# Performance work log

Hardware: AMD Instinct MI355X
Metric: run time of the kernel (lower is better)

## Reference

```python
import jax, jax.numpy as jnp
import numpy as np

B, N, C, D = 16, 1024, 768, 384

def setup_inputs() -> dict:
    key = jax.random.key(0)
    ks = jax.random.split(key, 12)
    s_in = 1.0 / np.sqrt(C)
    s_d = 1.0 / np.sqrt(D)
    return {
        "x": jax.random.normal(ks[0], (B, N, C), dtype=jnp.float32),
        "adj": jax.random.uniform(ks[1], (B, N, N), dtype=jnp.float32),
        "W_theta": jax.random.uniform(ks[2], (C, D), minval=-s_in, maxval=s_in),
        "b_theta": jax.random.uniform(ks[3], (D,), minval=-s_in, maxval=s_in),
        "W_phi": jax.random.uniform(ks[4], (C, D), minval=-s_in, maxval=s_in),
        "b_phi": jax.random.uniform(ks[5], (D,), minval=-s_in, maxval=s_in),
        "W_g": jax.random.uniform(ks[6], (C, D), minval=-s_in, maxval=s_in),
        "b_g": jax.random.uniform(ks[7], (D,), minval=-s_in, maxval=s_in),
        "W_out": jax.random.uniform(ks[8], (D, C), minval=-s_d, maxval=s_d),
        "b_out": jax.random.uniform(ks[9], (C,), minval=-s_d, maxval=s_d),
    }

def reference(x, adj, W_theta, b_theta, W_phi, b_phi, W_g, b_g, W_out, b_out):
    # projections: [B,N,C] @ [C,D] -> [B,N,D]
    theta = x @ W_theta + b_theta
    phi = x @ W_phi + b_phi
    g = x @ W_g + b_g
    # unscaled attention scores with multiplicative adjacency mask
    attn = jnp.einsum('bnd,bmd->bnm', theta, phi) * adj  # [B,N,N]
    attn = jax.nn.softmax(attn, axis=-1)  # dropout is identity in eval mode
    out = jnp.einsum('bnm,bmd->bnd', attn, g)  # [B,N,D]
    out = out @ W_out + b_out  # [B,N,C]
    return out + x
```

## Files before the change

kernel.cpp:

```cpp
#include <hip/hip_runtime.h>
#include <hip/hip_bf16.h>

typedef __hip_bfloat16 bf16;
typedef short bf16x8 __attribute__((ext_vector_type(8)));
typedef float f32x4 __attribute__((ext_vector_type(4)));

constexpr int Bb = 16, Nn = 1024, Cc = 768, Dd = 384;

static __device__ __forceinline__ f32x4 mfma16(bf16x8 a, bf16x8 b, f32x4 c) {
    return __builtin_amdgcn_mfma_f32_16x16x32_bf16(a, b, c, 0, 0, 0);
}
static __device__ __forceinline__ short f2b(float v) {
    __hip_bfloat16 h = __float2bfloat16(v);
    return *reinterpret_cast<short*>(&h);
}
static __device__ __forceinline__ unsigned pack2(float lo, float hi) {
    return ((unsigned)(unsigned short)f2b(hi) << 16) | (unsigned short)(unsigned)f2b(lo);
}
static __device__ __forceinline__ float b2f(bf16 x) { return __bfloat162float(x); }

__global__ __launch_bounds__(256) void cast_bf16(
    const float* __restrict__ in, uint4* __restrict__ out)
{
    const size_t i = (size_t)blockIdx.x * 256 + threadIdx.x;
    const float4 a = reinterpret_cast<const float4*>(in)[i * 2];
    const float4 b = reinterpret_cast<const float4*>(in)[i * 2 + 1];
    uint4 v;
    v.x = pack2(a.x, a.y);
    v.y = pack2(a.z, a.w);
    v.z = pack2(b.x, b.y);
    v.w = pack2(b.z, b.w);
    out[i] = v;
}

__global__ __launch_bounds__(256) void pack_bias(
    const float* __restrict__ bt, const float* __restrict__ bp,
    const float* __restrict__ bg, float* __restrict__ out)
{
    const int i = blockIdx.x * 256 + threadIdx.x;
    if (i < 384) out[i] = bt[i];
    else if (i < 768) out[i] = bp[i - 384];
    else if (i < 1152) out[i] = bg[i - 768];
}

__global__ __launch_bounds__(256) void transpose_cast(
    const float* __restrict__ in, bf16* __restrict__ out, int K, int N)
{
    __shared__ float t[32][33];
    const int n0 = blockIdx.x * 32, k0 = blockIdx.y * 32;
    const int tx = threadIdx.x & 31, ty = threadIdx.x >> 5;
#pragma unroll
    for (int i = 0; i < 4; i++)
        t[ty + i * 8][tx] = in[(size_t)(k0 + ty + i * 8) * N + n0 + tx];
    __syncthreads();
#pragma unroll
    for (int i = 0; i < 4; i++)
        out[(size_t)(n0 + ty + i * 8) * K + k0 + tx] = __float2bfloat16(t[tx][ty + i * 8]);
}

template <typename TA, int EPI>
__global__ __launch_bounds__(256) void gemm_mfma(
    const TA* __restrict__ A, const bf16* __restrict__ BT,
    const float* __restrict__ bias, const float* __restrict__ resid,
    void* __restrict__ outp, int K, int Nout)
{
    __shared__ short As[128 * 40];
    __shared__ short Bs[128 * 40];
    const int tid = threadIdx.x;
    const int lane = tid & 63, w = tid >> 6;
    const int quad = lane >> 4, c = lane & 15;
    const int row0 = blockIdx.x * 128, col0 = blockIdx.y * 128;
    const int wm = (w & 1) * 64, wn = (w >> 1) * 64;

    const f32x4 fz = {0.f, 0.f, 0.f, 0.f};
    f32x4 acc[4][4];
#pragma unroll
    for (int i = 0; i < 4; i++)
#pragma unroll
        for (int j = 0; j < 4; j++) acc[i][j] = fz;

    for (int k0 = 0; k0 < K; k0 += 32) {
        __syncthreads();
        if (sizeof(TA) == 4) {
            const float* Af = (const float*)A;
#pragma unroll
            for (int u = 0; u < 4; u++) {
                const int id = u * 256 + tid;
                const int r = id >> 3, c4 = (id & 7) * 4;
                const float4 v = *reinterpret_cast<const float4*>(Af + (size_t)(row0 + r) * K + k0 + c4);
                uint2 p;
                p.x = pack2(v.x, v.y);
                p.y = pack2(v.z, v.w);
                *reinterpret_cast<uint2*>(&As[r * 40 + c4]) = p;
            }
        } else {
            const bf16* Ab = (const bf16*)A;
#pragma unroll
            for (int u = 0; u < 2; u++) {
                const int id = u * 256 + tid;
                const int r = id >> 2, c8 = (id & 3) * 8;
                const uint4 v = *reinterpret_cast<const uint4*>(Ab + (size_t)(row0 + r) * K + k0 + c8);
                *reinterpret_cast<uint4*>(&As[r * 40 + c8]) = v;
            }
        }
#pragma unroll
        for (int u = 0; u < 2; u++) {
            const int id = u * 256 + tid;
            const int r = id >> 2, c8 = (id & 3) * 8;
            const uint4 v = *reinterpret_cast<const uint4*>(BT + (size_t)(col0 + r) * K + k0 + c8);
            *reinterpret_cast<uint4*>(&Bs[r * 40 + c8]) = v;
        }
        __syncthreads();

        bf16x8 af[4], bfr[4];
#pragma unroll
        for (int i = 0; i < 4; i++)
            af[i] = *reinterpret_cast<const bf16x8*>(&As[(wm + i * 16 + c) * 40 + quad * 8]);
#pragma unroll
        for (int j = 0; j < 4; j++)
            bfr[j] = *reinterpret_cast<const bf16x8*>(&Bs[(wn + j * 16 + c) * 40 + quad * 8]);
#pragma unroll
        for (int i = 0; i < 4; i++)
#pragma unroll
            for (int j = 0; j < 4; j++)
                acc[i][j] = mfma16(af[i], bfr[j], acc[i][j]);
    }

    const size_t SZc = (size_t)Bb * Nn * Dd;
#pragma unroll
    for (int i = 0; i < 4; i++) {
        const int rowb = row0 + wm + i * 16 + quad * 4;
#pragma unroll
        for (int j = 0; j < 4; j++) {
            const int col = col0 + wn + j * 16 + c;
            const float bcol = bias[col];
#pragma unroll
            for (int r = 0; r < 4; r++) {
                float v = acc[i][j][r] + bcol;
                const int rr = rowb + r;
                if (EPI == 0) {
                    ((bf16*)outp)[(size_t)rr * Nout + col] = __float2bfloat16(v);
                } else if (EPI == 1) {
                    const int bb = rr >> 10, m = rr & 1023;
                    ((bf16*)outp)[((size_t)(bb * Nout + col)) * 1024 + m] = __float2bfloat16(v);
                } else if (EPI == 2) {
                    v += resid[(size_t)rr * Nout + col];
                    ((float*)outp)[(size_t)rr * Nout + col] = v;
                } else {
                    const int seg = col / 384;
                    const int cl = col - seg * 384;
                    bf16* base = (bf16*)outp;
                    if (seg < 2) {
                        base[(size_t)seg * SZc + (size_t)rr * Dd + cl] = __float2bfloat16(v);
                    } else {
                        const int bb = rr >> 10, m = rr & 1023;
                        base[2 * SZc + ((size_t)(bb * Dd + cl)) * 1024 + m] = __float2bfloat16(v);
                    }
                }
            }
        }
    }
}

template <int SPLIT>
__global__ __launch_bounds__(256, 2) void flash_attn(
    const bf16* __restrict__ theta, const bf16* __restrict__ phi,
    const bf16* __restrict__ gT, const float* __restrict__ adj,
    bf16* __restrict__ O, float* __restrict__ Sp, float* __restrict__ ml)
{
    __shared__ short phs[32 * 392];
    __shared__ short gts[384 * 40];
    __shared__ short pls[4][16 * 40];

    const int tid = threadIdx.x;
    const int lane = tid & 63, w = tid >> 6;
    const int quad = lane >> 4, c = lane & 15;
    const int qb = blockIdx.x, b = blockIdx.y;
    const int sp = SPLIT ? blockIdx.z : 0;
    const int n_lo = SPLIT ? sp * (Nn / 2) : 0;
    const int n_hi = SPLIT ? n_lo + Nn / 2 : Nn;

    const size_t thbase = ((size_t)b * Nn + qb * 64 + w * 16 + c) * Dd;
    bf16x8 ath[12];
#pragma unroll
    for (int dq = 0; dq < 12; dq++)
        ath[dq] = *reinterpret_cast<const bf16x8*>(theta + thbase + dq * 32 + quad * 8);

    const f32x4 fz = {0.f, 0.f, 0.f, 0.f};
    f32x4 o[24];
#pragma unroll
    for (int t = 0; t < 24; t++) o[t] = fz;
    float mrow[4], lrow[4];
#pragma unroll
    for (int r = 0; r < 4; r++) { mrow[r] = -INFINITY; lrow[r] = 0.f; }

    for (int n0 = n_lo; n0 < n_hi; n0 += 32) {
        __syncthreads();
        {
            const bf16* src = phi + ((size_t)b * Nn + n0) * Dd;
#pragma unroll
            for (int u = 0; u < 6; u++) {
                const int id = u * 256 + tid;
                const int r = id / 48, cc = (id % 48) * 8;
                const uint4 v = *reinterpret_cast<const uint4*>(src + (size_t)r * Dd + cc);
                *reinterpret_cast<uint4*>(&phs[r * 392 + cc]) = v;
            }
        }
        {
            const bf16* src = gT + ((size_t)b * Dd) * Nn + n0;
#pragma unroll
            for (int u = 0; u < 6; u++) {
                const int id = u * 256 + tid;
                const int r = id >> 2, cc = (id & 3) * 8;
                const uint4 v = *reinterpret_cast<const uint4*>(src + (size_t)r * Nn + cc);
                *reinterpret_cast<uint4*>(&gts[r * 40 + cc]) = v;
            }
        }
        __syncthreads();

        f32x4 s0 = fz, s1 = fz;
#pragma unroll
        for (int dq = 0; dq < 12; dq++) {
            const bf16x8 b0 = *reinterpret_cast<const bf16x8*>(&phs[c * 392 + dq * 32 + quad * 8]);
            const bf16x8 b1 = *reinterpret_cast<const bf16x8*>(&phs[(16 + c) * 392 + dq * 32 + quad * 8]);
            s0 = mfma16(ath[dq], b0, s0);
            s1 = mfma16(ath[dq], b1, s1);
        }

        const float* arow = adj + ((size_t)b * Nn + qb * 64 + w * 16 + quad * 4) * Nn + n0;
        float p0[4], p1[4], alpha[4];
#pragma unroll
        for (int r = 0; r < 4; r++) {
            const float v0 = s0[r] * arow[(size_t)r * Nn + c];
            const float v1 = s1[r] * arow[(size_t)r * Nn + 16 + c];
            float t = fmaxf(v0, v1);
#pragma unroll
            for (int msk = 1; msk < 16; msk <<= 1) t = fmaxf(t, __shfl_xor(t, msk));
            const float mn = fmaxf(mrow[r], t);
            alpha[r] = __expf(mrow[r] - mn);
            mrow[r] = mn;
            p0[r] = __expf(v0 - mn);
            p1[r] = __expf(v1 - mn);
            float u = p0[r] + p1[r];
#pragma unroll
            for (int msk = 1; msk < 16; msk <<= 1) u += __shfl_xor(u, msk);
            lrow[r] = lrow[r] * alpha[r] + u;
        }
#pragma unroll
        for (int t = 0; t < 24; t++)
#pragma unroll
            for (int r = 0; r < 4; r++) o[t][r] *= alpha[r];

        short* pl = (short*)pls[w];
#pragma unroll
        for (int r = 0; r < 4; r++) {
            pl[(quad * 4 + r) * 40 + c] = f2b(p0[r]);
            pl[(quad * 4 + r) * 40 + 16 + c] = f2b(p1[r]);
        }
        __syncthreads();
        const bf16x8 ap = *reinterpret_cast<const bf16x8*>(&pl[c * 40 + quad * 8]);
#pragma unroll
        for (int dn = 0; dn < 24; dn++) {
            const bf16x8 bg = *reinterpret_cast<const bf16x8*>(&gts[(dn * 16 + c) * 40 + quad * 8]);
            o[dn] = mfma16(ap, bg, o[dn]);
        }
    }

    const int rowb = qb * 64 + w * 16 + quad * 4;
    if (SPLIT) {
        float* srow = Sp + ((size_t)sp * Bb * Nn + (size_t)b * Nn + rowb) * Dd;
#pragma unroll
        for (int dn = 0; dn < 24; dn++)
#pragma unroll
            for (int r = 0; r < 4; r++)
                srow[(size_t)r * Dd + dn * 16 + c] = o[dn][r];
        if (c == 0) {
#pragma unroll
            for (int r = 0; r < 4; r++) {
                const size_t rid = (size_t)sp * Bb * Nn + (size_t)b * Nn + rowb + r;
                ml[rid * 2]     = mrow[r];
                ml[rid * 2 + 1] = lrow[r];
            }
        }
    } else {
        float inv[4];
#pragma unroll
        for (int r = 0; r < 4; r++) inv[r] = 1.0f / lrow[r];
        bf16* orow = O + ((size_t)b * Nn + rowb) * Dd;
#pragma unroll
        for (int dn = 0; dn < 24; dn++)
#pragma unroll
            for (int r = 0; r < 4; r++)
                orow[(size_t)r * Dd + dn * 16 + c] = __float2bfloat16(o[dn][r] * inv[r]);
    }
}

__global__ __launch_bounds__(256) void attn_combine(
    const float* __restrict__ Sp, const float* __restrict__ ml,
    bf16* __restrict__ O)
{
    constexpr size_t M = (size_t)Bb * Nn;
    const size_t idx = (size_t)blockIdx.x * 256 + threadIdx.x;
    const size_t e0 = idx * 4;
    const size_t row = e0 / Dd;
    const float m1 = ml[row * 2],           l1 = ml[row * 2 + 1];
    const float m2 = ml[(M + row) * 2],     l2 = ml[(M + row) * 2 + 1];
    const float mx = fmaxf(m1, m2);
    const float w1 = __expf(m1 - mx), w2 = __expf(m2 - mx);
    const float inv = 1.0f / (w1 * l1 + w2 * l2);
    const float4 a = *reinterpret_cast<const float4*>(Sp + e0);
    const float4 b = *reinterpret_cast<const float4*>(Sp + M * Dd + e0);
    uint2 p;
    p.x = pack2((w1 * a.x + w2 * b.x) * inv, (w1 * a.y + w2 * b.y) * inv);
    p.y = pack2((w1 * a.z + w2 * b.z) * inv, (w1 * a.w + w2 * b.w) * inv);
    *reinterpret_cast<uint2*>(O + e0) = p;
}

__global__ __launch_bounds__(256) void proj_gemm(
    const float* __restrict__ A, const float* __restrict__ W,
    const float* __restrict__ bias, bf16* __restrict__ out,
    int M, int K, int Nd)
{
    __shared__ float Asm[16][65];
    __shared__ float Bsm[16][65];
    const int tid = threadIdx.x;
    const int tx = tid & 15, ty = tid >> 4;
    const int row0 = blockIdx.x * 64, col0 = blockIdx.y * 64;
    float acc[4][4] = {};
    for (int k0 = 0; k0 < K; k0 += 16) {
        {
            const int m = tid >> 2, kq = (tid & 3) * 4;
            const float* p = A + (size_t)(row0 + m) * K + k0 + kq;
#pragma unroll
            for (int j = 0; j < 4; j++) Asm[kq + j][m] = p[j];
        }
        {
            const int k = tid >> 4, n4 = (tid & 15) * 4;
            const float* p = W + (size_t)(k0 + k) * Nd + col0 + n4;
#pragma unroll
            for (int j = 0; j < 4; j++) Bsm[k][n4 + j] = p[j];
        }
        __syncthreads();
#pragma unroll
        for (int k = 0; k < 16; k++) {
            float a[4], bv[4];
#pragma unroll
            for (int j = 0; j < 4; j++) a[j] = Asm[k][ty * 4 + j];
#pragma unroll
            for (int j = 0; j < 4; j++) bv[j] = Bsm[k][tx * 4 + j];
#pragma unroll
            for (int i = 0; i < 4; i++)
#pragma unroll
                for (int j = 0; j < 4; j++) acc[i][j] += a[i] * bv[j];
        }
        __syncthreads();
    }
#pragma unroll
    for (int i = 0; i < 4; i++) {
        const int row = row0 + ty * 4 + i;
#pragma unroll
        for (int j = 0; j < 4; j++) {
            const int col = col0 + tx * 4 + j;
            out[(size_t)row * Nd + col] = __float2bfloat16(acc[i][j] + bias[col]);
        }
    }
}

__global__ __launch_bounds__(256) void fused_attn(
    const float* __restrict__ x, const float* __restrict__ adj,
    const float* __restrict__ W_theta, const float* __restrict__ b_theta,
    const bf16* __restrict__ phi, const bf16* __restrict__ g,
    const float* __restrict__ W_out, const float* __restrict__ b_out,
    float* __restrict__ out)
{
    __shared__ float xs[Cc];
    __shared__ float th[Dd];
    __shared__ float s[Nn];
    __shared__ float Os[Dd];
    __shared__ float red[256];
    const int tid = threadIdx.x;
    const int n = blockIdx.x, b = blockIdx.y;
    const int lane = tid & 63, wave = tid >> 6;
    const size_t row = (size_t)b * Nn + n;
    const size_t baseD = (size_t)b * Nn * Dd;
    for (int c = tid; c < Cc; c += 256) xs[c] = x[row * Cc + c];
    __syncthreads();
    for (int d = tid; d < Dd; d += 256) {
        float acc = b_theta[d];
#pragma unroll 8
        for (int c = 0; c < Cc; c++) acc += xs[c] * W_theta[(size_t)c * Dd + d];
        th[d] = acc;
    }
    __syncthreads();
    for (int m = wave; m < Nn; m += 4) {
        const bf16* prow = phi + baseD + (size_t)m * Dd;
        float partial = 0.f;
#pragma unroll
        for (int j = 0; j < 6; j++) {
            const int d = lane + 64 * j;
            partial += th[d] * b2f(prow[d]);
        }
#pragma unroll
        for (int off = 32; off > 0; off >>= 1) partial += __shfl_down(partial, off);
        if (lane == 0)
            s[m] = partial * adj[(size_t)b * Nn * Nn + (size_t)n * Nn + m];
    }
    __syncthreads();
    float mx = -1e30f;
    for (int i = tid; i < Nn; i += 256) mx = fmaxf(mx, s[i]);
    red[tid] = mx; __syncthreads();
    for (int st = 128; st > 0; st >>= 1) {
        if (tid < st) red[tid] = fmaxf(red[tid], red[tid + st]);
        __syncthreads();
    }
    mx = red[0]; __syncthreads();
    float lsum = 0.f;
    for (int i = tid; i < Nn; i += 256) {
        const float e = __expf(s[i] - mx);
        s[i] = e;
        lsum += e;
    }
    red[tid] = lsum; __syncthreads();
    for (int st = 128; st > 0; st >>= 1) {
        if (tid < st) red[tid] += red[tid + st];
        __syncthreads();
    }
    const float inv = 1.0f / red[0];
    __syncthreads();
    for (int d = tid; d < Dd; d += 256) {
        float acc = 0.f;
#pragma unroll 8
        for (int m = 0; m < Nn; m++) acc += s[m] * b2f(g[baseD + (size_t)m * Dd + d]);
        Os[d] = acc * inv;
    }
    __syncthreads();
    for (int c = tid; c < Cc; c += 256) {
        float acc = b_out[c] + xs[c];
#pragma unroll 8
        for (int d = 0; d < Dd; d++) acc += Os[d] * W_out[(size_t)d * Cc + c];
        out[row * Cc + c] = acc;
    }
}

extern "C" void kernel_launch(void* const* d_in, const int* in_sizes, int n_in,
                              void* d_out, int out_size, void* d_ws, size_t ws_size,
                              hipStream_t stream)
{
    const float* x       = (const float*)d_in[0];
    const float* adj     = (const float*)d_in[1];
    const float* W_theta = (const float*)d_in[2];
    const float* b_theta = (const float*)d_in[3];
    const float* W_phi   = (const float*)d_in[4];
    const float* b_phi   = (const float*)d_in[5];
    const float* W_g     = (const float*)d_in[6];
    const float* b_g     = (const float*)d_in[7];
    const float* W_out   = (const float*)d_in[8];
    const float* b_out   = (const float*)d_in[9];
    float* out = (float*)d_out;

    const int M = Bb * Nn;
    const size_t SZ  = (size_t)Bb * Nn * Dd;
    const size_t SZX = (size_t)M * Cc;
    const size_t WSZ = (size_t)Cc * Dd;
    const size_t NEED_OLD = (4 * WSZ + 4 * SZ) * sizeof(bf16);
    const size_t NEED_NEW = (4 * WSZ + 4 * SZ + SZX) * sizeof(bf16)
                          + 1152 * sizeof(float);
    const size_t NEED_SPLIT = NEED_NEW
                          + (2 * SZ + 4 * (size_t)M) * sizeof(float);

    dim3 blk(256);

    if (ws_size >= NEED_NEW) {
        bf16* WtT   = (bf16*)d_ws;
        bf16* WpT   = WtT + WSZ;
        bf16* WgT   = WpT + WSZ;
        bf16* WoT   = WgT + WSZ;
        bf16* theta = WoT + WSZ;
        bf16* phi   = theta + SZ;
        bf16* gT    = phi + SZ;
        bf16* O     = gT + SZ;
        bf16* xb    = O + SZ;
        float* biasP = (float*)(xb + SZX);
        float* Sp    = biasP + 1152;
        float* mlp   = Sp + 2 * SZ;

        cast_bf16<<<dim3((unsigned)(SZX / 2048)), blk, 0, stream>>>(x, (uint4*)xb);
        transpose_cast<<<dim3(Dd / 32, Cc / 32), blk, 0, stream>>>(W_theta, WtT, Cc, Dd);
        transpose_cast<<<dim3(Dd / 32, Cc / 32), blk, 0, stream>>>(W_phi,   WpT, Cc, Dd);
        transpose_cast<<<dim3(Dd / 32, Cc / 32), blk, 0, stream>>>(W_g,     WgT, Cc, Dd);
        transpose_cast<<<dim3(Cc / 32, Dd / 32), blk, 0, stream>>>(W_out,   WoT, Dd, Cc);
        pack_bias<<<dim3(5), blk, 0, stream>>>(b_theta, b_phi, b_g, biasP);

        gemm_mfma<bf16, 3><<<dim3(M / 128, 1152 / 128), blk, 0, stream>>>(
            xb, WtT, biasP, nullptr, theta, Cc, 1152);

        if (ws_size >= NEED_SPLIT) {
            flash_attn<1><<<dim3(Nn / 64, Bb, 2), blk, 0, stream>>>(
                theta, phi, gT, adj, nullptr, Sp, mlp);
            attn_combine<<<dim3((unsigned)(SZ / 1024)), blk, 0, stream>>>(Sp, mlp, O);
        } else {
            flash_attn<0><<<dim3(Nn / 64, Bb, 1), blk, 0, stream>>>(
                theta, phi, gT, adj, O, nullptr, nullptr);
        }

        gemm_mfma<bf16, 2><<<dim3(M / 128, Cc / 128), blk, 0, stream>>>(
            O, WoT, b_out, x, out, Dd, Cc);
    } else if (ws_size >= NEED_OLD) {
        bf16* WtT   = (bf16*)d_ws;
        bf16* WpT   = WtT + WSZ;
        bf16* WgT   = WpT + WSZ;
        bf16* WoT   = WgT + WSZ;
        bf16* theta = WoT + WSZ;
        bf16* phi   = theta + SZ;
        bf16* gT    = phi + SZ;
        bf16* O     = gT + SZ;

        transpose_cast<<<dim3(Dd / 32, Cc / 32), blk, 0, stream>>>(W_theta, WtT, Cc, Dd);
        transpose_cast<<<dim3(Dd / 32, Cc / 32), blk, 0, stream>>>(W_phi,   WpT, Cc, Dd);
        transpose_cast<<<dim3(Dd / 32, Cc / 32), blk, 0, stream>>>(W_g,     WgT, Cc, Dd);
        transpose_cast<<<dim3(Cc / 32, Dd / 32), blk, 0, stream>>>(W_out,   WoT, Dd, Cc);

        dim3 gp(M / 128, Dd / 128);
        gemm_mfma<float, 0><<<gp, blk, 0, stream>>>(x, WtT, b_theta, nullptr, theta, Cc, Dd);
        gemm_mfma<float, 0><<<gp, blk, 0, stream>>>(x, WpT, b_phi,   nullptr, phi,   Cc, Dd);
        gemm_mfma<float, 1><<<gp, blk, 0, stream>>>(x, WgT, b_g,     nullptr, gT,    Cc, Dd);

        flash_attn<0><<<dim3(Nn / 64, Bb, 1), blk, 0, stream>>>(
            theta, phi, gT, adj, O, nullptr, nullptr);

        dim3 go(M / 128, Cc / 128);
        gemm_mfma<bf16, 2><<<go, blk, 0, stream>>>(O, WoT, b_out, x, out, Dd, Cc);
    } else {
        bf16* phi = (bf16*)d_ws;
        bf16* g   = phi + SZ;
        dim3 gproj(M / 64, Dd / 64);
        proj_gemm<<<gproj, blk, 0, stream>>>(x, W_phi, b_phi, phi, M, Cc, Dd);
        proj_gemm<<<gproj, blk, 0, stream>>>(x, W_g, b_g, g, M, Cc, Dd);
        fused_attn<<<dim3(Nn, Bb), blk, 0, stream>>>(
            x, adj, W_theta, b_theta, phi, g, W_out, b_out, out);
    }
}
```

Before: 341.8 us.

## Split attention KV into four chunks, shrink LDS, swizzle gT tile, fuse prep kernels

The flash attention kernel now splits the key range four ways instead of two, and attn_combine is generalised to merge NS partial results. Shared memory shrinks: the per-warp P scratch reuses the phi buffer, and the gT tile uses a compact XOR-swizzled layout. Both changes are meant to allow three blocks per CU and to reduce LDS bank conflicts. The small prep kernels (x cast plus bias pack, and the three weight transposes) are merged to cut launch count. In exchange the split writes and re-reads twice as much fp32 partial output, and an extra __syncthreads is added before the P stores.

```diff
diff --git a/kernel.cpp b/kernel.cpp
--- a/kernel.cpp
+++ b/kernel.cpp
@@ -19,8 +19,10 @@
 }
 static __device__ __forceinline__ float b2f(bf16 x) { return __bfloat162float(x); }
 
-__global__ __launch_bounds__(256) void cast_bf16(
-    const float* __restrict__ in, uint4* __restrict__ out)
+__global__ __launch_bounds__(256) void cast_bias(
+    const float* __restrict__ in, uint4* __restrict__ out,
+    const float* __restrict__ bt, const float* __restrict__ bp,
+    const float* __restrict__ bg, float* __restrict__ biasP)
 {
     const size_t i = (size_t)blockIdx.x * 256 + threadIdx.x;
     const float4 a = reinterpret_cast<const float4*>(in)[i * 2];
@@ -31,16 +33,10 @@
     v.z = pack2(b.x, b.y);
     v.w = pack2(b.z, b.w);
     out[i] = v;
-}
-
-__global__ __launch_bounds__(256) void pack_bias(
-    const float* __restrict__ bt, const float* __restrict__ bp,
-    const float* __restrict__ bg, float* __restrict__ out)
-{
-    const int i = blockIdx.x * 256 + threadIdx.x;
-    if (i < 384) out[i] = bt[i];
-    else if (i < 768) out[i] = bp[i - 384];
-    else if (i < 1152) out[i] = bg[i - 768];
+    if (blockIdx.x == 0) {
+        for (int k = threadIdx.x; k < 1152; k += 256)
+            biasP[k] = k < 384 ? bt[k] : (k < 768 ? bp[k - 384] : bg[k - 768]);
+    }
 }
 
 __global__ __launch_bounds__(256) void transpose_cast(
@@ -56,6 +52,24 @@
 #pragma unroll
     for (int i = 0; i < 4; i++)
         out[(size_t)(n0 + ty + i * 8) * K + k0 + tx] = __float2bfloat16(t[tx][ty + i * 8]);
+}
+
+__global__ __launch_bounds__(256) void transpose_cast3(
+    const float* __restrict__ w0, const float* __restrict__ w1,
+    const float* __restrict__ w2, bf16* __restrict__ outbase)
+{
+    __shared__ float t[32][33];
+    const float* in = blockIdx.z == 0 ? w0 : (blockIdx.z == 1 ? w1 : w2);
+    bf16* out = outbase + (size_t)blockIdx.z * Cc * Dd;
+    const int n0 = blockIdx.x * 32, k0 = blockIdx.y * 32;
+    const int tx = threadIdx.x & 31, ty = threadIdx.x >> 5;
+#pragma unroll
+    for (int i = 0; i < 4; i++)
+        t[ty + i * 8][tx] = in[(size_t)(k0 + ty + i * 8) * Dd + n0 + tx];
+    __syncthreads();
+#pragma unroll
+    for (int i = 0; i < 4; i++)
+        out[(size_t)(n0 + ty + i * 8) * Cc + k0 + tx] = __float2bfloat16(t[tx][ty + i * 8]);
 }
 
 template <typename TA, int EPI>
@@ -163,22 +177,21 @@
 }
 
 template <int SPLIT>
-__global__ __launch_bounds__(256, 2) void flash_attn(
+__global__ __launch_bounds__(256, 3) void flash_attn(
     const bf16* __restrict__ theta, const bf16* __restrict__ phi,
     const bf16* __restrict__ gT, const float* __restrict__ adj,
     bf16* __restrict__ O, float* __restrict__ Sp, float* __restrict__ ml)
 {
     __shared__ short phs[32 * 392];
-    __shared__ short gts[384 * 40];
-    __shared__ short pls[4][16 * 40];
+    __shared__ short gts[192 * 64];
 
     const int tid = threadIdx.x;
     const int lane = tid & 63, w = tid >> 6;
     const int quad = lane >> 4, c = lane & 15;
     const int qb = blockIdx.x, b = blockIdx.y;
-    const int sp = SPLIT ? blockIdx.z : 0;
-    const int n_lo = SPLIT ? sp * (Nn / 2) : 0;
-    const int n_hi = SPLIT ? n_lo + Nn / 2 : Nn;
+    const int sp = (SPLIT > 1) ? blockIdx.z : 0;
+    constexpr int CH = Nn / SPLIT;
+    const int n_lo = sp * CH;
 
     const size_t thbase = ((size_t)b * Nn + qb * 64 + w * 16 + c) * Dd;
     bf16x8 ath[12];
@@ -186,6 +199,8 @@
     for (int dq = 0; dq < 12; dq++)
         ath[dq] = *reinterpret_cast<const bf16x8*>(theta + thbase + dq * 32 + quad * 8);
 
+    const int goff = (c >> 1) * 64 + (((4 * (c & 1) + quad) ^ ((c >> 1) & 7)) * 8);
+
     const f32x4 fz = {0.f, 0.f, 0.f, 0.f};
     f32x4 o[24];
 #pragma unroll
@@ -194,7 +209,8 @@
 #pragma unroll
     for (int r = 0; r < 4; r++) { mrow[r] = -INFINITY; lrow[r] = 0.f; }
 
-    for (int n0 = n_lo; n0 < n_hi; n0 += 32) {
+    for (int it = 0; it < CH / 32; ++it) {
+        const int n0 = n_lo + it * 32;
         __syncthreads();
         {
             const bf16* src = phi + ((size_t)b * Nn + n0) * Dd;
@@ -211,9 +227,11 @@
 #pragma unroll
             for (int u = 0; u < 6; u++) {
                 const int id = u * 256 + tid;
-                const int r = id >> 2, cc = (id & 3) * 8;
-                const uint4 v = *reinterpret_cast<const uint4*>(src + (size_t)r * Nn + cc);
-                *reinterpret_cast<uint4*>(&gts[r * 40 + cc]) = v;
+                const int r = id >> 3, sl = id & 7;
+                const int sg = sl ^ (r & 7);
+                const int d = 2 * r + (sg >> 2), cc = (sg & 3) * 8;
+                const uint4 v = *reinterpret_cast<const uint4*>(src + (size_t)d * Nn + cc);
+                *reinterpret_cast<uint4*>(&gts[id * 8]) = v;
             }
         }
         __syncthreads();
@@ -251,23 +269,23 @@
 #pragma unroll
             for (int r = 0; r < 4; r++) o[t][r] *= alpha[r];
 
-        short* pl = (short*)pls[w];
+        __syncthreads();
+        short* pl = phs + w * 640;
 #pragma unroll
         for (int r = 0; r < 4; r++) {
             pl[(quad * 4 + r) * 40 + c] = f2b(p0[r]);
             pl[(quad * 4 + r) * 40 + 16 + c] = f2b(p1[r]);
         }
-        __syncthreads();
         const bf16x8 ap = *reinterpret_cast<const bf16x8*>(&pl[c * 40 + quad * 8]);
 #pragma unroll
         for (int dn = 0; dn < 24; dn++) {
-            const bf16x8 bg = *reinterpret_cast<const bf16x8*>(&gts[(dn * 16 + c) * 40 + quad * 8]);
+            const bf16x8 bg = *reinterpret_cast<const bf16x8*>(&gts[dn * 512 + goff]);
             o[dn] = mfma16(ap, bg, o[dn]);
         }
     }
 
     const int rowb = qb * 64 + w * 16 + quad * 4;
-    if (SPLIT) {
+    if (SPLIT > 1) {
         float* srow = Sp + ((size_t)sp * Bb * Nn + (size_t)b * Nn + rowb) * Dd;
 #pragma unroll
         for (int dn = 0; dn < 24; dn++)
@@ -295,6 +313,7 @@
     }
 }
 
+template <int NS>
 __global__ __launch_bounds__(256) void attn_combine(
     const float* __restrict__ Sp, const float* __restrict__ ml,
     bf16* __restrict__ O)
@@ -303,16 +322,27 @@
     const size_t idx = (size_t)blockIdx.x * 256 + threadIdx.x;
     const size_t e0 = idx * 4;
     const size_t row = e0 / Dd;
-    const float m1 = ml[row * 2],           l1 = ml[row * 2 + 1];
-    const float m2 = ml[(M + row) * 2],     l2 = ml[(M + row) * 2 + 1];
-    const float mx = fmaxf(m1, m2);
-    const float w1 = __expf(m1 - mx), w2 = __expf(m2 - mx);
-    const float inv = 1.0f / (w1 * l1 + w2 * l2);
-    const float4 a = *reinterpret_cast<const float4*>(Sp + e0);
-    const float4 b = *reinterpret_cast<const float4*>(Sp + M * Dd + e0);
+    float mv[NS], lv[NS];
+    float mx = -INFINITY;
+#pragma unroll
+    for (int i = 0; i < NS; i++) {
+        mv[i] = ml[((size_t)i * M + row) * 2];
+        lv[i] = ml[((size_t)i * M + row) * 2 + 1];
+        mx = fmaxf(mx, mv[i]);
+    }
+    float wsum = 0.f, wv[NS];
+#pragma unroll
+    for (int i = 0; i < NS; i++) { wv[i] = __expf(mv[i] - mx); wsum += wv[i] * lv[i]; }
+    const float inv = 1.0f / wsum;
+    float ax = 0.f, ay = 0.f, az = 0.f, aw = 0.f;
+#pragma unroll
+    for (int i = 0; i < NS; i++) {
+        const float4 a = *reinterpret_cast<const float4*>(Sp + (size_t)i * M * Dd + e0);
+        ax += wv[i] * a.x; ay += wv[i] * a.y; az += wv[i] * a.z; aw += wv[i] * a.w;
+    }
     uint2 p;
-    p.x = pack2((w1 * a.x + w2 * b.x) * inv, (w1 * a.y + w2 * b.y) * inv);
-    p.y = pack2((w1 * a.z + w2 * b.z) * inv, (w1 * a.w + w2 * b.w) * inv);
+    p.x = pack2(ax * inv, ay * inv);
+    p.y = pack2(az * inv, aw * inv);
     *reinterpret_cast<uint2*>(O + e0) = p;
 }
 
@@ -465,16 +495,14 @@
     const size_t NEED_OLD = (4 * WSZ + 4 * SZ) * sizeof(bf16);
     const size_t NEED_NEW = (4 * WSZ + 4 * SZ + SZX) * sizeof(bf16)
                           + 1152 * sizeof(float);
-    const size_t NEED_SPLIT = NEED_NEW
-                          + (2 * SZ + 4 * (size_t)M) * sizeof(float);
+    const size_t NEED_S2 = NEED_NEW + (2 * SZ + 4 * (size_t)M) * sizeof(float);
+    const size_t NEED_S4 = NEED_NEW + (4 * SZ + 8 * (size_t)M) * sizeof(float);
 
     dim3 blk(256);
 
     if (ws_size >= NEED_NEW) {
         bf16* WtT   = (bf16*)d_ws;
-        bf16* WpT   = WtT + WSZ;
-        bf16* WgT   = WpT + WSZ;
-        bf16* WoT   = WgT + WSZ;
+        bf16* WoT   = WtT + 3 * WSZ;
         bf16* theta = WoT + WSZ;
         bf16* phi   = theta + SZ;
         bf16* gT    = phi + SZ;
@@ -482,24 +510,28 @@
         bf16* xb    = O + SZ;
         float* biasP = (float*)(xb + SZX);
         float* Sp    = biasP + 1152;
-        float* mlp   = Sp + 2 * SZ;
-
-        cast_bf16<<<dim3((unsigned)(SZX / 2048)), blk, 0, stream>>>(x, (uint4*)xb);
-        transpose_cast<<<dim3(Dd / 32, Cc / 32), blk, 0, stream>>>(W_theta, WtT, Cc, Dd);
-        transpose_cast<<<dim3(Dd / 32, Cc / 32), blk, 0, stream>>>(W_phi,   WpT, Cc, Dd);
-        transpose_cast<<<dim3(Dd / 32, Cc / 32), blk, 0, stream>>>(W_g,     WgT, Cc, Dd);
-        transpose_cast<<<dim3(Cc / 32, Dd / 32), blk, 0, stream>>>(W_out,   WoT, Dd, Cc);
-        pack_bias<<<dim3(5), blk, 0, stream>>>(b_theta, b_phi, b_g, biasP);
+        float* mlp   = Sp + 4 * SZ;
+
+        cast_bias<<<dim3((unsigned)(SZX / 2048)), blk, 0, stream>>>(
+            x, (uint4*)xb, b_theta, b_phi, b_g, biasP);
+        transpose_cast3<<<dim3(Dd / 32, Cc / 32, 3), blk, 0, stream>>>(
+            W_theta, W_phi, W_g, WtT);
+        transpose_cast<<<dim3(Cc / 32, Dd / 32), blk, 0, stream>>>(W_out, WoT, Dd, Cc);
 
         gemm_mfma<bf16, 3><<<dim3(M / 128, 1152 / 128), blk, 0, stream>>>(
             xb, WtT, biasP, nullptr, theta, Cc, 1152);
 
-        if (ws_size >= NEED_SPLIT) {
-            flash_attn<1><<<dim3(Nn / 64, Bb, 2), blk, 0, stream>>>(
+        if (ws_size >= NEED_S4) {
+            flash_attn<4><<<dim3(Nn / 64, Bb, 4), blk, 0, stream>>>(
                 theta, phi, gT, adj, nullptr, Sp, mlp);
-            attn_combine<<<dim3((unsigned)(SZ / 1024)), blk, 0, stream>>>(Sp, mlp, O);
+            attn_combine<4><<<dim3((unsigned)(SZ / 1024)), blk, 0, stream>>>(Sp, mlp, O);
+        } else if (ws_size >= NEED_S2) {
+            float* mlp2 = Sp + 2 * SZ;
+            flash_attn<2><<<dim3(Nn / 64, Bb, 2), blk, 0, stream>>>(
+                theta, phi, gT, adj, nullptr, Sp, mlp2);
+            attn_combine<2><<<dim3((unsigned)(SZ / 1024)), blk, 0, stream>>>(Sp, mlp2, O);
         } else {
-            flash_attn<0><<<dim3(Nn / 64, Bb, 1), blk, 0, stream>>>(
+            flash_attn<1><<<dim3(Nn / 64, Bb, 1), blk, 0, stream>>>(
                 theta, phi, gT, adj, O, nullptr, nullptr);
         }
 
@@ -508,8 +540,8 @@
     } else if (ws_size >= NEED_OLD) {
         bf16* WtT   = (bf16*)d_ws;
         bf16* WpT   = WtT + WSZ;
-        bf16* WgT   = WpT + WSZ;
-        bf16* WoT   = WgT + WSZ;
+        bf16* WgT   = WtT + 2 * WSZ;
+        bf16* WoT   = WtT + 3 * WSZ;
         bf16* theta = WoT + WSZ;
         bf16* phi   = theta + SZ;
         bf16* gT    = phi + SZ;
@@ -525,7 +557,7 @@
         gemm_mfma<float, 0><<<gp, blk, 0, stream>>>(x, WpT, b_phi,   nullptr, phi,   Cc, Dd);
         gemm_mfma<float, 1><<<gp, blk, 0, stream>>>(x, WgT, b_g,     nullptr, gT,    Cc, Dd);
 
-        flash_attn<0><<<dim3(Nn / 64, Bb, 1), blk, 0, stream>>>(
+        flash_attn<1><<<dim3(Nn / 64, Bb, 1), blk, 0, stream>>>(
             theta, phi, gT, adj, O, nullptr, nullptr);
 
         dim3 go(M / 128, Cc / 128);
```

Measured after the change: 496.3 us. +45.2%, slower.
